# Kernel optimization log

Measured on AMD Instinct MI355X. Metric: run time of the kernel, lower is better.

Reference implementation:

```python
import jax, jax.numpy as jnp
import numpy as np

N, E = 50000, 800000
IN_F, OUT_F = 256, 128


def setup_inputs() -> dict:
    key = jax.random.key(0)
    ks = jax.random.split(key, 12)
    s = 1.0 / np.sqrt(OUT_F)
    si = 1.0 / np.sqrt(IN_F)
    return {
        "h": jax.random.normal(ks[0], (N, IN_F), jnp.float32),
        "degrees": jax.random.randint(ks[1], (E, 6), 0, 5).astype(jnp.float32),
        "norm": jax.random.uniform(ks[2], (N, 1), jnp.float32, 0.05, 1.0),
        "src": jax.random.randint(ks[3], (E,), 0, N, jnp.int32),
        "dst": jax.random.randint(ks[4], (E,), 0, N, jnp.int32),
        "W_self": jax.random.normal(ks[5], (IN_F, OUT_F), jnp.float32) * si,
        "b_self": jax.random.normal(ks[6], (OUT_F,), jnp.float32) * si,
        "W_node": jax.random.normal(ks[7], (IN_F, 6 * OUT_F), jnp.float32) * si,
        "b_node": jax.random.normal(ks[8], (6 * OUT_F,), jnp.float32) * si,
        "W_edge": jax.random.normal(ks[9], (6, OUT_F), jnp.float32) * 0.4,
        "bias": jax.random.normal(ks[10], (1, OUT_F), jnp.float32) * 2 * s - s,
    }


def reference(h, degrees, norm, src, dst, W_self, b_self, W_node, b_node, W_edge, bias):
    n = h.shape[0]
    out = W_self.shape[1]
    # node-level linears
    h_node_msg = (h @ W_node + b_node).reshape(n, 6, out)  # [N,6,out]
    h_node_self = h @ W_self + b_self                       # [N,out]
    # edge-level linear (no bias)
    msg = degrees @ W_edge                                  # [E,out]
    mask = (degrees > 0).astype(h.dtype)                    # [E,6]
    # masked sum over the 6 degree-conditioned slices (gather per slice to
    # avoid materializing an [E,6,out] tensor)
    for i in range(6):
        msg = msg + h_node_msg[src, i] * mask[:, i:i + 1]
    msg = msg * norm[src]                                   # src-side norm
    accum = jax.ops.segment_sum(msg, dst, num_segments=n) * norm  # dst-side norm
    return jax.nn.relu(accum + h_node_self + bias)
```

## Files before the change

### kernel.cpp

```cpp
#include <hip/hip_runtime.h>
#include <stdint.h>

#define IN_F 256
#define OUT_F 128
#define NCOLS 1024
#define PROWB 1152
#define BM 64
#define BN 128
#define BK 32

using bf16x8 = __attribute__((ext_vector_type(8))) __bf16;
using f32x4  = __attribute__((ext_vector_type(4))) float;
using f32x2  = __attribute__((ext_vector_type(2))) float;

static __device__ __forceinline__ unsigned short f2bf(float f) {
    unsigned u = __float_as_uint(f);
    u = u + 0x7fffu + ((u >> 16) & 1u);
    return (unsigned short)(u >> 16);
}
static __device__ __forceinline__ float bf_lo(unsigned u) { return __uint_as_float(u << 16); }
static __device__ __forceinline__ float bf_hi(unsigned u) { return __uint_as_float(u & 0xffff0000u); }

static __device__ __forceinline__ void async_load16(const void* g, void* l) {
    __builtin_amdgcn_global_load_lds(
        (__attribute__((address_space(1))) void*)g,
        (__attribute__((address_space(3))) void*)l,
        16, 0, 0);
}

__global__ void k_conv_h(const float* __restrict__ h, unsigned short* __restrict__ hb, int total8) {
    int i = blockIdx.x * blockDim.x + threadIdx.x;
    if (i >= total8) return;
    const float4* src = ((const float4*)h) + (size_t)i * 2;
    float4 a = src[0], b = src[1];
    union { unsigned short us[8]; uint4 v; } u;
    u.us[0] = f2bf(a.x); u.us[1] = f2bf(a.y); u.us[2] = f2bf(a.z); u.us[3] = f2bf(a.w);
    u.us[4] = f2bf(b.x); u.us[5] = f2bf(b.y); u.us[6] = f2bf(b.z); u.us[7] = f2bf(b.w);
    ((uint4*)hb)[i] = u.v;
}

__global__ void k_conv_w(const float* __restrict__ Wn, const float* __restrict__ Ws,
                         const float* __restrict__ bn, const float* __restrict__ bs,
                         unsigned short* __restrict__ Wt, float* __restrict__ bvec, int total) {
    int i = blockIdx.x * blockDim.x + threadIdx.x;
    if (i >= total) return;
    int k = i >> 10, c = i & 1023;
    float v;
    if (c < 768) {
        v = Wn[(size_t)k * 768 + c];
    } else if (c < 896) {
        int j = c - 768; v = 0.f;
#pragma unroll
        for (int s = 0; s < 6; ++s) v += Wn[(size_t)k * 768 + s * 128 + j];
    } else {
        v = Ws[(size_t)k * 128 + (c - 896)];
    }
    Wt[(size_t)c * IN_F + k] = f2bf(v);

    if (i < NCOLS) {
        float b;
        if (i < 768) b = bn[i];
        else if (i < 896) {
            int j = i - 768; b = 0.f;
#pragma unroll
            for (int s = 0; s < 6; ++s) b += bn[s * 128 + j];
        } else b = bs[i - 896];
        bvec[i] = b;
    }
}

__global__ void __launch_bounds__(256) k_gemm(
    const unsigned short* __restrict__ hb,
    const unsigned short* __restrict__ Wt,
    const float* __restrict__ bvec,
    const float* __restrict__ norm,
    char* __restrict__ PG, int N, int rowsPerXcd)
{
    __shared__ char lds[(BM + BN) * BK * 2];
    __shared__ unsigned short Pst[BM * BN];
    char* Ab = lds;
    char* Bb = lds + BM * BK * 2;

    const int f  = blockIdx.x;
    const int xc = f & 7;
    const int j  = f >> 3;
    const int rs = xc * rowsPerXcd + (j >> 3);
    const int ct = j & 7;
    const int r0 = rs * BM;
    if (r0 >= N) return;
    const int c0 = ct * BN;

    const int tid = threadIdx.x;
    const int wid = tid >> 6, lane = tid & 63;
    const int lrow = lane & 15, s = lane >> 4;
    const int wr = wid >> 1, wc = wid & 1;

    const int arow = tid >> 2;
    const int achunk = (tid & 3) ^ ((arow >> 1) & 3);
    int agrow = r0 + arow; if (agrow >= N) agrow = N - 1;
    const unsigned short* aseg = hb + (size_t)agrow * IN_F + achunk * 8;

    const int bcol0 = tid >> 2;
    const int bchunk0 = (tid & 3) ^ ((bcol0 >> 1) & 3);
    const unsigned short* bseg0 = Wt + (size_t)(c0 + bcol0) * IN_F + bchunk0 * 8;
    const int idx1 = tid + 256;
    const int bcol1 = idx1 >> 2;
    const int bchunk1 = (idx1 & 3) ^ ((bcol1 >> 1) & 3);
    const unsigned short* bseg1 = Wt + (size_t)(c0 + bcol1) * IN_F + bchunk1 * 8;

    int a_off[2], b_off[4];
#pragma unroll
    for (int m = 0; m < 2; ++m) {
        int rl = wr * 32 + m * 16 + lrow;
        a_off[m] = rl * 64 + ((s ^ ((rl >> 1) & 3)) << 4);
    }
#pragma unroll
    for (int n = 0; n < 4; ++n) {
        int cl = wc * 64 + n * 16 + lrow;
        b_off[n] = cl * 64 + ((s ^ ((cl >> 1) & 3)) << 4);
    }

    float nrmv[2][4];
#pragma unroll
    for (int m = 0; m < 2; ++m)
#pragma unroll
        for (int r = 0; r < 4; ++r) {
            int rg = r0 + wr * 32 + m * 16 + s * 4 + r;
            nrmv[m][r] = norm[rg < N ? rg : N - 1];
        }

    f32x4 acc[2][4] = {};

    for (int kk = 0; kk < IN_F / BK; ++kk) {
        async_load16(aseg + kk * BK, Ab + tid * 16);
        async_load16(bseg0 + kk * BK, Bb + tid * 16);
        async_load16(bseg1 + kk * BK, Bb + (tid + 256) * 16);
        __syncthreads();

        bf16x8 af[2], bfv[4];
#pragma unroll
        for (int m = 0; m < 2; ++m) af[m] = *(const bf16x8*)(Ab + a_off[m]);
#pragma unroll
        for (int n = 0; n < 4; ++n) bfv[n] = *(const bf16x8*)(Bb + b_off[n]);
#pragma unroll
        for (int m = 0; m < 2; ++m)
#pragma unroll
            for (int n = 0; n < 4; ++n)
                acc[m][n] = __builtin_amdgcn_mfma_f32_16x16x32_bf16(af[m], bfv[n], acc[m][n], 0, 0, 0);
        __syncthreads();
    }

    float bvn[4];
#pragma unroll
    for (int n = 0; n < 4; ++n) bvn[n] = bvec[c0 + wc * 64 + n * 16 + lrow];

    if (ct < 7) {
        char* PstB = (char*)Pst;
#pragma unroll
        for (int m = 0; m < 2; ++m) {
            const int rowl = wr * 32 + m * 16 + s * 4;
#pragma unroll
            for (int n = 0; n < 4; ++n) {
#pragma unroll
                for (int r = 0; r < 4; ++r) {
                    float v = (acc[m][n][r] + bvn[n]) * nrmv[m][r];
                    int pk = __builtin_amdgcn_cvt_pk_fp8_f32(v, v, 0, false);
                    const int row = rowl + r;
                    PstB[row * 128 + (((wc * 4 + n) ^ (row & 7)) * 16) + lrow] = (char)pk;
                }
            }
        }
        __syncthreads();
#pragma unroll
        for (int it = 0; it < 2; ++it) {
            const int idx = it * 256 + tid;
            const int rl = idx >> 3, ch = idx & 7;
            const int rg = r0 + rl;
            if (rg < N) {
                uint4 v = *(const uint4*)&PstB[rl * 128 + ((ch ^ (rl & 7)) * 16)];
                *(uint4*)(PG + (size_t)rg * PROWB + ct * 128 + ch * 16) = v;
            }
        }
    } else {
#pragma unroll
        for (int m = 0; m < 2; ++m) {
            const int rowl = wr * 32 + m * 16 + s * 4;
#pragma unroll
            for (int n = 0; n < 4; ++n) {
                const int col = wc * 64 + n * 16 + lrow;
                const int chunk = col >> 3, cb = col & 7;
#pragma unroll
                for (int r = 0; r < 4; ++r) {
                    float v = acc[m][n][r] + bvn[n];
                    const int row = rowl + r;
                    Pst[row * 128 + ((chunk ^ (row & 7)) * 8 + cb)] = f2bf(v);
                }
            }
        }
        __syncthreads();
        const int ch = tid & 15;
#pragma unroll
        for (int rr = 0; rr < 4; ++rr) {
            const int rl = rr * 16 + (tid >> 4);
            const int rg = r0 + rl;
            if (rg < N) {
                uint4 v = *(const uint4*)&Pst[rl * 128 + ((ch ^ (rl & 7)) * 8)];
                *(uint4*)(PG + (size_t)rg * PROWB + 896 + ch * 16) = v;
            }
        }
    }
}

__global__ void k_hist(const int* __restrict__ dst, int* __restrict__ counts, int E) {
    int e = blockIdx.x * blockDim.x + threadIdx.x;
    if (e < E) atomicAdd(&counts[dst[e]], 1);
}

__global__ void __launch_bounds__(256) k_scan_a(const int* __restrict__ counts,
                                                int* __restrict__ offs,
                                                int* __restrict__ bsum, int N) {
    __shared__ int sm[256];
    int tid = threadIdx.x;
    int i = blockIdx.x * 256 + tid;
    int v = (i < N) ? counts[i] : 0;
    sm[tid] = v;
    __syncthreads();
#pragma unroll
    for (int st = 1; st < 256; st <<= 1) {
        int t = (tid >= st) ? sm[tid - st] : 0;
        __syncthreads();
        sm[tid] += t;
        __syncthreads();
    }
    if (i < N) offs[i] = sm[tid] - v;
    if (tid == 255) bsum[blockIdx.x] = sm[255];
}

__global__ void __launch_bounds__(256) k_scan_b(int* __restrict__ bsum, int NB) {
    __shared__ int sm[256];
    int tid = threadIdx.x;
    int v = (tid < NB) ? bsum[tid] : 0;
    sm[tid] = v;
    __syncthreads();
#pragma unroll
    for (int st = 1; st < 256; st <<= 1) {
        int t = (tid >= st) ? sm[tid - st] : 0;
        __syncthreads();
        sm[tid] += t;
        __syncthreads();
    }
    if (tid < NB) bsum[tid] = sm[tid] - v;
}

__global__ void k_scan_c(int* __restrict__ offs, const int* __restrict__ bsum,
                         int* __restrict__ cursor, int N) {
    int i = blockIdx.x * 256 + threadIdx.x;
    if (i >= N) return;
    int o = offs[i] + bsum[blockIdx.x];
    offs[i] = o;
    cursor[i] = o;
}

__global__ void k_scatter(const int* __restrict__ src, const int* __restrict__ dst,
                          const float* __restrict__ degrees,
                          int* __restrict__ cursor, uint2* __restrict__ pedge, int E) {
    int e = blockIdx.x * blockDim.x + threadIdx.x;
    if (e >= E) return;
    int d = dst[e];
    int slot = atomicAdd(&cursor[d], 1);
    unsigned pk = 0;
#pragma unroll
    for (int i = 0; i < 6; ++i) {
        float df = degrees[(size_t)e * 6 + i];
        pk |= ((unsigned)df) << (4 * i);
    }
    pedge[slot] = make_uint2((unsigned)src[e], pk);
}

__global__ void __launch_bounds__(256) k_aggregate(
    const char* __restrict__ PG,
    const int* __restrict__ row_start, const int* __restrict__ counts,
    const uint2* __restrict__ pedge,
    const float* __restrict__ norm, const float* __restrict__ W_edge,
    const float* __restrict__ bias, float* __restrict__ out, int N)
{
    __shared__ unsigned EL[4][192];
    const int wid = threadIdx.x >> 6;
    const int n = blockIdx.x * 4 + wid;
    if (n >= N) return;
    const int lane = threadIdx.x & 63;
    const int l2 = lane * 2;
    unsigned* el = EL[wid];

    float2 w[6];
#pragma unroll
    for (int i = 0; i < 6; ++i) w[i] = *(const float2*)(W_edge + i * OUT_F + lane * 2);

    const int beg = row_start[n];
    const int end = beg + counts[n];

    float Swd[6] = {0.f, 0.f, 0.f, 0.f, 0.f, 0.f};
    float g0 = 0.f, g1 = 0.f;

    for (int p0 = beg; p0 < end; p0 += 64) {
        const int t = p0 + lane;
        uint2 pe = (t < end) ? pedge[t] : make_uint2(0u, 0u);
        const unsigned dp = pe.y;
        const float nr = (dp != 0u) ? norm[pe.x] : 0.f;

        unsigned zm = 0;
#pragma unroll
        for (int i = 0; i < 6; ++i) {
            int d = (dp >> (4 * i)) & 15;
            if (d == 0) zm |= (1u << i);
            Swd[i] += nr * (float)d;
        }
        const int z = __popc(zm);
        const int ne = (dp == 0u) ? 0 : ((z <= 2) ? (1 + z) : (6 - z));

        int x = ne;
#pragma unroll
        for (int st = 1; st < 64; st <<= 1) {
            int v = __shfl_up(x, st);
            if (lane >= st) x += v;
        }
        const int excl = x - ne;
        const int total = __shfl(x, 63);

        if (ne) {
            const unsigned base = pe.x * (unsigned)PROWB;
            int wp = excl;
            if (z <= 2) {
                el[wp++] = base + 768u;
#pragma unroll
                for (int i = 0; i < 6; ++i)
                    if ((zm >> i) & 1u) el[wp++] = (base + i * 128u) | 0x80000000u;
            } else {
#pragma unroll
                for (int i = 0; i < 6; ++i)
                    if (!((zm >> i) & 1u)) el[wp++] = base + i * 128u;
            }
        }
        asm volatile("s_waitcnt lgkmcnt(0)" ::: "memory");

        int j = 0;
        for (; j + 8 <= total; j += 8) {
            unsigned ev[8];
            unsigned short qv[8];
#pragma unroll
            for (int q = 0; q < 8; ++q)
                ev[q] = __builtin_amdgcn_readfirstlane(el[j + q]);
#pragma unroll
            for (int q = 0; q < 8; ++q)
                qv[q] = *(const unsigned short*)(PG + (ev[q] & 0x7fffffffu) + l2);
#pragma unroll
            for (int q = 0; q < 8; ++q) {
                f32x2 fq = __builtin_amdgcn_cvt_pk_f32_fp8((int)qv[q], false);
                float sg = __uint_as_float(0x3f800000u | (ev[q] & 0x80000000u));
                g0 = fmaf(sg, fq.x, g0);
                g1 = fmaf(sg, fq.y, g1);
            }
        }
        for (; j < total; ++j) {
            unsigned e0 = __builtin_amdgcn_readfirstlane(el[j]);
            unsigned short q0 = *(const unsigned short*)(PG + (e0 & 0x7fffffffu) + l2);
            f32x2 f0 = __builtin_amdgcn_cvt_pk_f32_fp8((int)q0, false);
            float sg = __uint_as_float(0x3f800000u | (e0 & 0x80000000u));
            g0 = fmaf(sg, f0.x, g0);
            g1 = fmaf(sg, f0.y, g1);
        }
    }

    float b0 = 0.f, b1 = 0.f;
#pragma unroll
    for (int i = 0; i < 6; ++i) {
        float v = Swd[i];
#pragma unroll
        for (int st = 1; st < 64; st <<= 1) v += __shfl_xor(v, st);
        b0 = fmaf(v, w[i].x, b0);
        b1 = fmaf(v, w[i].y, b1);
    }

    const unsigned us = *(const unsigned*)(PG + (size_t)n * PROWB + 896 + lane * 4);
    const float nd = norm[n];
    const float2 bv = *(const float2*)(bias + lane * 2);
    float2 o;
    o.x = fmaxf((g0 + b0) * nd + bf_lo(us) + bv.x, 0.f);
    o.y = fmaxf((g1 + b1) * nd + bf_hi(us) + bv.y, 0.f);
    *(float2*)(out + (size_t)n * OUT_F + lane * 2) = o;
}

extern "C" void kernel_launch(void* const* d_in, const int* in_sizes, int n_in,
                              void* d_out, int out_size, void* d_ws, size_t ws_size,
                              hipStream_t stream)
{
    const float* h       = (const float*)d_in[0];
    const float* degrees = (const float*)d_in[1];
    const float* norm    = (const float*)d_in[2];
    const int*   src     = (const int*)d_in[3];
    const int*   dst     = (const int*)d_in[4];
    const float* W_self  = (const float*)d_in[5];
    const float* b_self  = (const float*)d_in[6];
    const float* W_node  = (const float*)d_in[7];
    const float* b_node  = (const float*)d_in[8];
    const float* W_edge  = (const float*)d_in[9];
    const float* bias    = (const float*)d_in[10];
    float* out = (float*)d_out;

    const int N = in_sizes[2];
    const int E = in_sizes[3];
    const int NB = (N + 255) / 256;

    char* ws = (char*)d_ws;
    size_t off = 0;
    auto alloc = [&](size_t sz) { size_t o = off; off = (off + sz + 255) & ~(size_t)255; return o; };
    char*           PG     = (char*)(ws + alloc((size_t)N * PROWB));
    unsigned short* hb     = (unsigned short*)(ws + alloc((size_t)N * IN_F * 2));
    unsigned short* Wt     = (unsigned short*)(ws + alloc((size_t)NCOLS * IN_F * 2));
    float*          bvec   = (float*)(ws + alloc(NCOLS * 4));
    int*            counts = (int*)(ws + alloc((size_t)N * 4));
    int*            offs   = (int*)(ws + alloc((size_t)N * 4));
    int*            cursor = (int*)(ws + alloc((size_t)N * 4));
    int*            bsum   = (int*)(ws + alloc((size_t)NB * 4));
    uint2*          pedge  = (uint2*)(ws + alloc((size_t)E * 8));

    hipMemsetAsync(counts, 0, (size_t)N * 4, stream);

    int t8 = N * (IN_F / 8);
    k_conv_h<<<(t8 + 255) / 256, 256, 0, stream>>>(h, hb, t8);

    int tw = IN_F * NCOLS;
    k_conv_w<<<(tw + 255) / 256, 256, 0, stream>>>(W_node, W_self, b_node, b_self, Wt, bvec, tw);

    const int R  = (N + BM - 1) / BM;
    const int RP = (R + 7) / 8;
    k_gemm<<<RP * 8 * 8, 256, 0, stream>>>(hb, Wt, bvec, norm, PG, N, RP);

    k_hist<<<(E + 255) / 256, 256, 0, stream>>>(dst, counts, E);
    k_scan_a<<<NB, 256, 0, stream>>>(counts, offs, bsum, N);
    k_scan_b<<<1, 256, 0, stream>>>(bsum, NB);
    k_scan_c<<<NB, 256, 0, stream>>>(offs, bsum, cursor, N);
    k_scatter<<<(E + 255) / 256, 256, 0, stream>>>(src, dst, degrees, cursor, pedge, E);

    k_aggregate<<<(N + 3) / 4, 256, 0, stream>>>(PG, offs, counts, pedge,
                                                 norm, W_edge, bias, out, N);
}
```

Measured before the change: 210.3 us.

## Store GEMM epilogue directly to global in MFMA-native column permutation

```diff
diff --git a/kernel.cpp b/kernel.cpp
--- a/kernel.cpp
+++ b/kernel.cpp
@@ -77,7 +77,6 @@
     char* __restrict__ PG, int N, int rowsPerXcd)
 {
     __shared__ char lds[(BM + BN) * BK * 2];
-    __shared__ unsigned short Pst[BM * BN];
     char* Ab = lds;
     char* Bb = lds + BM * BK * 2;
 
@@ -155,57 +154,37 @@
     for (int n = 0; n < 4; ++n) bvn[n] = bvec[c0 + wc * 64 + n * 16 + lrow];
 
     if (ct < 7) {
-        char* PstB = (char*)Pst;
 #pragma unroll
         for (int m = 0; m < 2; ++m) {
-            const int rowl = wr * 32 + m * 16 + s * 4;
-#pragma unroll
-            for (int n = 0; n < 4; ++n) {
-#pragma unroll
-                for (int r = 0; r < 4; ++r) {
-                    float v = (acc[m][n][r] + bvn[n]) * nrmv[m][r];
-                    int pk = __builtin_amdgcn_cvt_pk_fp8_f32(v, v, 0, false);
-                    const int row = rowl + r;
-                    PstB[row * 128 + (((wc * 4 + n) ^ (row & 7)) * 16) + lrow] = (char)pk;
-                }
+#pragma unroll
+            for (int r = 0; r < 4; ++r) {
+                const int rg = r0 + wr * 32 + m * 16 + s * 4 + r;
+                if (rg >= N) continue;
+                const float sc = nrmv[m][r];
+                float v0 = (acc[m][0][r] + bvn[0]) * sc;
+                float v1 = (acc[m][1][r] + bvn[1]) * sc;
+                float v2 = (acc[m][2][r] + bvn[2]) * sc;
+                float v3 = (acc[m][3][r] + bvn[3]) * sc;
+                int pk = __builtin_amdgcn_cvt_pk_fp8_f32(v0, v1, 0, false);
+                pk = __builtin_amdgcn_cvt_pk_fp8_f32(v2, v3, pk, true);
+                *(int*)(PG + (size_t)rg * PROWB + ct * 128 + (wc * 16 + lrow) * 4) = pk;
             }
         }
-        __syncthreads();
-#pragma unroll
-        for (int it = 0; it < 2; ++it) {
-            const int idx = it * 256 + tid;
-            const int rl = idx >> 3, ch = idx & 7;
-            const int rg = r0 + rl;
-            if (rg < N) {
-                uint4 v = *(const uint4*)&PstB[rl * 128 + ((ch ^ (rl & 7)) * 16)];
-                *(uint4*)(PG + (size_t)rg * PROWB + ct * 128 + ch * 16) = v;
-            }
-        }
     } else {
 #pragma unroll
         for (int m = 0; m < 2; ++m) {
-            const int rowl = wr * 32 + m * 16 + s * 4;
-#pragma unroll
-            for (int n = 0; n < 4; ++n) {
-                const int col = wc * 64 + n * 16 + lrow;
-                const int chunk = col >> 3, cb = col & 7;
-#pragma unroll
-                for (int r = 0; r < 4; ++r) {
-                    float v = acc[m][n][r] + bvn[n];
-                    const int row = rowl + r;
-                    Pst[row * 128 + ((chunk ^ (row & 7)) * 8 + cb)] = f2bf(v);
-                }
-            }
-        }
-        __syncthreads();
-        const int ch = tid & 15;
-#pragma unroll
-        for (int rr = 0; rr < 4; ++rr) {
-            const int rl = rr * 16 + (tid >> 4);
-            const int rg = r0 + rl;
-            if (rg < N) {
-                uint4 v = *(const uint4*)&Pst[rl * 128 + ((ch ^ (rl & 7)) * 8)];
-                *(uint4*)(PG + (size_t)rg * PROWB + 896 + ch * 16) = v;
+#pragma unroll
+            for (int r = 0; r < 4; ++r) {
+                const int rg = r0 + wr * 32 + m * 16 + s * 4 + r;
+                if (rg >= N) continue;
+                float v0 = acc[m][0][r] + bvn[0];
+                float v1 = acc[m][1][r] + bvn[1];
+                float v2 = acc[m][2][r] + bvn[2];
+                float v3 = acc[m][3][r] + bvn[3];
+                uint2 dd;
+                dd.x = (unsigned)f2bf(v0) | ((unsigned)f2bf(v1) << 16);
+                dd.y = (unsigned)f2bf(v2) | ((unsigned)f2bf(v3) << 16);
+                *(uint2*)(PG + (size_t)rg * PROWB + 896 + (wc * 32 + 2 * lrow) * 4) = dd;
             }
         }
     }
@@ -292,9 +271,15 @@
     const int l2 = lane * 2;
     unsigned* el = EL[wid];
 
-    float2 w[6];
-#pragma unroll
-    for (int i = 0; i < 6; ++i) w[i] = *(const float2*)(W_edge + i * OUT_F + lane * 2);
+    const int cA = (lane >> 5) * 64 + (lane & 1) * 32 + ((lane >> 1) & 15);
+    const int cB = cA + 16;
+
+    float wA[6], wB[6];
+#pragma unroll
+    for (int i = 0; i < 6; ++i) {
+        wA[i] = W_edge[i * OUT_F + cA];
+        wB[i] = W_edge[i * OUT_F + cB];
+    }
 
     const int beg = row_start[n];
     const int end = beg + counts[n];
@@ -377,17 +362,16 @@
         float v = Swd[i];
 #pragma unroll
         for (int st = 1; st < 64; st <<= 1) v += __shfl_xor(v, st);
-        b0 = fmaf(v, w[i].x, b0);
-        b1 = fmaf(v, w[i].y, b1);
+        b0 = fmaf(v, wA[i], b0);
+        b1 = fmaf(v, wB[i], b1);
     }
 
     const unsigned us = *(const unsigned*)(PG + (size_t)n * PROWB + 896 + lane * 4);
     const float nd = norm[n];
-    const float2 bv = *(const float2*)(bias + lane * 2);
-    float2 o;
-    o.x = fmaxf((g0 + b0) * nd + bf_lo(us) + bv.x, 0.f);
-    o.y = fmaxf((g1 + b1) * nd + bf_hi(us) + bv.y, 0.f);
-    *(float2*)(out + (size_t)n * OUT_F + lane * 2) = o;
+    float o0 = fmaxf((g0 + b0) * nd + bf_lo(us) + bias[cA], 0.f);
+    float o1 = fmaxf((g1 + b1) * nd + bf_hi(us) + bias[cB], 0.f);
+    out[(size_t)n * OUT_F + cA] = o0;
+    out[(size_t)n * OUT_F + cB] = o1;
 }
 
 extern "C" void kernel_launch(void* const* d_in, const int* in_sizes, int n_in,
```

Measured after the change: 210.8 us. No clear change (+0.2%).
